# Kernel tuning notes

Hardware: AMD Instinct MI355X
Metric: run time of the kernel (lower is better)

Reference implementation:

```python
import jax, jax.numpy as jnp
import numpy as np


def setup_inputs() -> dict:
    key = jax.random.key(0)
    ks = jax.random.split(key, 8)
    B, C, H, W, D = 2, 128, 16, 16, 16
    C8 = C // 8
    return {
        "x": jax.random.normal(ks[0], (B, C, H, W, D), dtype=jnp.float32),
        "wq": jax.random.normal(ks[1], (C8, C), dtype=jnp.float32) * (1.0 / np.sqrt(C)),
        "bq": jax.random.normal(ks[2], (C8,), dtype=jnp.float32) * 0.02,
        "wk": jax.random.normal(ks[3], (C8, C), dtype=jnp.float32) * (1.0 / np.sqrt(C)),
        "bk": jax.random.normal(ks[4], (C8,), dtype=jnp.float32) * 0.02,
        "wv": jax.random.normal(ks[5], (C, C), dtype=jnp.float32) * (1.0 / np.sqrt(C)),
        "bv": jax.random.normal(ks[6], (C,), dtype=jnp.float32) * 0.02,
        "gamma": jax.random.normal(ks[7], (1,), dtype=jnp.float32) * 0.1,
    }


def reference(x, wq, bq, wk, bk, wv, bv, gamma):
    B, C, H, W, D = x.shape
    N = H * W * D
    xf = x.reshape(B, C, N)                      # (B, C, N) flatten H,W,D
    # 1x1x1 convs == per-voxel linear over channels
    q = jnp.einsum('oc,bcn->bon', wq, xf) + bq[None, :, None]   # (B, C//8, N)
    k = jnp.einsum('oc,bcn->bon', wk, xf) + bk[None, :, None]   # (B, C//8, N)
    v = jnp.einsum('oc,bcn->bon', wv, xf) + bv[None, :, None]   # (B, C, N)
    # energy[b, i, j] = sum_c q[b,c,i] * k[b,c,j]  (no scaling, as in source)
    energy = jnp.einsum('bci,bcj->bij', q, k)                   # (B, N, N)
    attn = jax.nn.softmax(energy, axis=-1)
    # out[b,c,i] = sum_j v[b,c,j] * attn[b,i,j]
    out = jnp.einsum('bcj,bij->bci', v, attn)                   # (B, C, N)
    out = out.reshape(B, C, H, W, D)
    return gamma[0] * out + x
```

## Files before the change

kernel.cpp:

```cpp
#include <hip/hip_runtime.h>
#include <hip/hip_bf16.h>
#include <math.h>

#define N_VOX 4096

typedef __bf16 bf16x8 __attribute__((ext_vector_type(8)));
typedef __bf16 bf16x4 __attribute__((ext_vector_type(4)));
typedef float f32x4 __attribute__((ext_vector_type(4)));

#define QT_OFF  0
#define KT_OFF  524288
#define VP_OFF  1048576

#define P_LN8 2.0794415f

__device__ __forceinline__ f32x4 mfma16(f32x4 a, f32x4 b, f32x4 c) {
  return __builtin_amdgcn_mfma_f32_16x16x32_bf16(
      __builtin_bit_cast(bf16x8, a), __builtin_bit_cast(bf16x8, b), c, 0, 0, 0);
}
__device__ __forceinline__ void pin(f32x4& v) { asm volatile("" : "+v"(v)); }
__device__ __forceinline__ void pinl(long& v) { asm volatile("" : "+v"(v)); }

__device__ __forceinline__ unsigned f32_to_fp8x4(float a, float b, float c, float d) {
  int v = __builtin_amdgcn_cvt_pk_fp8_f32(a, b, 0, false);
  v = __builtin_amdgcn_cvt_pk_fp8_f32(c, d, v, true);
  return (unsigned)v;
}
__device__ __forceinline__ unsigned char f32_to_fp8(float a) {
  return (unsigned char)(__builtin_amdgcn_cvt_pk_fp8_f32(a, a, 0, false) & 0xff);
}

__global__ __launch_bounds__(256) void proj_kernel(
    const float* __restrict__ x,
    const float* __restrict__ wq, const float* __restrict__ bq,
    const float* __restrict__ wk, const float* __restrict__ bk,
    const float* __restrict__ wv, const float* __restrict__ bv,
    unsigned char* __restrict__ ws8) {
  __shared__ __bf16 xs[32 * 136];
  __shared__ __bf16 wb[160 * 136];

  const int t   = threadIdx.x;
  const int bid = blockIdx.x;
  const int b   = bid >> 7;
  const int n0  = (bid & 127) * 32;

  for (int i = t; i < 5120; i += 256) {
    int gid = i * 4;
    const float* src = (gid < 2048) ? wq + gid
                     : (gid < 4096) ? wk + (gid - 2048)
                                    : wv + (gid - 4096);
    float4 f = *reinterpret_cast<const float4*>(src);
    int r = gid >> 7, col = gid & 127;
    bf16x4 o;
    o[0] = (__bf16)f.x; o[1] = (__bf16)f.y; o[2] = (__bf16)f.z; o[3] = (__bf16)f.w;
    *reinterpret_cast<bf16x4*>(&wb[r * 136 + col]) = o;
  }
  for (int idx = t; idx < 128 * 8; idx += 256) {
    int c = idx >> 3, v4 = idx & 7;
    float4 xv = *reinterpret_cast<const float4*>(
        x + (size_t)(b * 128 + c) * N_VOX + n0 + v4 * 4);
    xs[(v4 * 4 + 0) * 136 + c] = (__bf16)xv.x;
    xs[(v4 * 4 + 1) * 136 + c] = (__bf16)xv.y;
    xs[(v4 * 4 + 2) * 136 + c] = (__bf16)xv.z;
    xs[(v4 * 4 + 3) * 136 + c] = (__bf16)xv.w;
  }
  __syncthreads();

  const int w = t >> 6, lane = t & 63;
  const int cq = lane & 15, g = lane >> 4, g8 = g * 8, g4 = g * 4;

  __bf16* qt = reinterpret_cast<__bf16*>(ws8 + QT_OFF);
  __bf16* kt = reinterpret_cast<__bf16*>(ws8 + KT_OFF);
  unsigned char* vp = ws8 + VP_OFF;
  const f32x4 zero4 = {0.f, 0.f, 0.f, 0.f};

  for (int ot = w; ot < 10; ot += 4) {
    int wrow = (ot == 0) ? cq : (ot == 1) ? 16 + cq : 32 + (ot - 2) * 16 + cq;
    const float* bias = (ot == 0) ? bq : (ot == 1) ? bk : bv + (ot - 2) * 16;

    f32x4 acc[2] = {zero4, zero4};
#pragma unroll
    for (int ks = 0; ks < 4; ++ks) {
      bf16x8 af = *reinterpret_cast<const bf16x8*>(&wb[wrow * 136 + ks * 32 + g8]);
#pragma unroll
      for (int nf = 0; nf < 2; ++nf) {
        bf16x8 bfr = *reinterpret_cast<const bf16x8*>(
            &xs[(nf * 16 + cq) * 136 + ks * 32 + g8]);
        acc[nf] = __builtin_amdgcn_mfma_f32_16x16x32_bf16(af, bfr, acc[nf], 0, 0, 0);
      }
    }

    float4 bl = *reinterpret_cast<const float4*>(bias + g4);
    const float* blp = reinterpret_cast<const float*>(&bl);
#pragma unroll
    for (int nf = 0; nf < 2; ++nf) {
      int n = n0 + nf * 16 + cq;
#pragma unroll
      for (int v = 0; v < 4; ++v) {
        float val = acc[nf][v] + blp[v];
        int o = g4 + v;
        if (ot == 0) {
          qt[(size_t)(b * 4096 + n) * 32 + o] = (__bf16)val;
          qt[(size_t)(b * 4096 + n) * 32 + 16 + o] = (__bf16)0.f;
        } else if (ot == 1) {
          kt[(size_t)(b * 4096 + n) * 32 + o] = (__bf16)val;
          kt[(size_t)(b * 4096 + n) * 32 + 16 + o] = (__bf16)0.f;
        } else {
          int c  = (ot - 2) * 16 + o;
          int jt = n >> 6, j_in = n & 63;
          int cn = j_in >> 5, gg = (j_in & 31) >> 3, e = j_in & 7;
          int lt = (c & 15) | (gg << 4);
          vp[((((size_t)b * 64 + jt) * 8 + (c >> 4)) * 2 + cn) * 512 + lt * 8 + e]
              = f32_to_fp8(val);
        }
      }
    }
  }
}

__global__ __launch_bounds__(512, 2) void attn_kernel(
    const unsigned char* __restrict__ ws8,
    const float* __restrict__ x,
    const float* __restrict__ gamma_p,
    float* __restrict__ out) {
  __shared__ __align__(16) unsigned char ps[8][32 * 72];
  __shared__ float o_lds[4][128][33];
  __shared__ float m_lds[8][32], l_lds[8][32], lstar_lds[32];

  const int t    = threadIdx.x;
  const int w    = t >> 6;
  const int lane = t & 63;
  const int cq   = lane & 15;
  const int g    = lane >> 4;
  const int g8   = g * 8;
  const int g4   = g * 4;

  const int raw = blockIdx.x;
  const int xcd = raw & 7;
  const int b   = xcd >> 2;
  const int qt0 = ((raw >> 3) * 4 + (xcd & 3)) * 32;

  const __bf16* qt = reinterpret_cast<const __bf16*>(ws8 + QT_OFF);
  const __bf16* kt = reinterpret_cast<const __bf16*>(ws8 + KT_OFF);
  const unsigned char* vp = ws8 + VP_OFF;

  f32x4 qfrag[2];
#pragma unroll
  for (int qf = 0; qf < 2; ++qf)
    qfrag[qf] = *reinterpret_cast<const f32x4*>(
        qt + (size_t)(b * 4096 + qt0 + qf * 16 + cq) * 32 + g8);

  const f32x4 zero4 = {0.f, 0.f, 0.f, 0.f};
  f32x4 acc[8][2];
#pragma unroll
  for (int ct = 0; ct < 8; ++ct) { acc[ct][0] = zero4; acc[ct][1] = zero4; }
  float m0 = -1e30f, m1 = -1e30f, l0 = 0.f, l1 = 0.f;

  unsigned char* psw0 = &ps[w][cq * 72];
  unsigned char* psw1 = &ps[w][(16 + cq) * 72];
  const __bf16* kbase = kt + (size_t)(b * 4096 + cq) * 32 + g8;
  const unsigned char* vbase = vp + (size_t)b * 524288 + lane * 8;

  const int jt_base = w * 8;

  f32x4 kf[4];
#pragma unroll
  for (int s = 0; s < 4; ++s)
    kf[s] = *reinterpret_cast<const f32x4*>(
        kbase + (size_t)(jt_base * 64 + s * 16) * 32);

#pragma unroll 1
  for (int tile = 0; tile < 8; ++tile) {
    const int jt = jt_base + tile;
    const int jn = jt_base + ((tile + 1) & 7);

    long vf[2][8];
#pragma unroll
    for (int cn = 0; cn < 2; ++cn)
#pragma unroll
      for (int ct = 0; ct < 8; ++ct)
        vf[cn][ct] = *reinterpret_cast<const long*>(
            vbase + ((((size_t)jt * 8 + ct) * 2 + cn) << 9));
    f32x4 kn[4];
#pragma unroll
    for (int s = 0; s < 4; ++s)
      kn[s] = *reinterpret_cast<const f32x4*>(
          kbase + (size_t)(jn * 64 + s * 16) * 32);

    f32x4 sf[4][2];
#pragma unroll
    for (int s = 0; s < 4; ++s) {
      sf[s][0] = mfma16(kf[s], qfrag[0], zero4);
      sf[s][1] = mfma16(kf[s], qfrag[1], zero4);
    }

    float tmax0 = sf[0][0][0], tmax1 = sf[0][1][0];
#pragma unroll
    for (int s = 0; s < 4; ++s)
#pragma unroll
      for (int v = 0; v < 4; ++v) {
        tmax0 = fmaxf(tmax0, sf[s][0][v]);
        tmax1 = fmaxf(tmax1, sf[s][1][v]);
      }
    tmax0 = fmaxf(tmax0, __shfl_xor(tmax0, 16));
    tmax0 = fmaxf(tmax0, __shfl_xor(tmax0, 32));
    tmax1 = fmaxf(tmax1, __shfl_xor(tmax1, 16));
    tmax1 = fmaxf(tmax1, __shfl_xor(tmax1, 32));

    if (__any((tmax0 > m0 + 8.0f) || (tmax1 > m1 + 8.0f))) {
      float m0n = fmaxf(m0, tmax0), m1n = fmaxf(m1, tmax1);
      float sc0 = __expf(m0 - m0n), sc1 = __expf(m1 - m1n);
#pragma unroll
      for (int ct = 0; ct < 8; ++ct) { acc[ct][0] *= sc0; acc[ct][1] *= sc1; }
      l0 *= sc0; l1 *= sc1;
      m0 = m0n; m1 = m1n;
    }

    float psum0 = 0.f, psum1 = 0.f;
#pragma unroll
    for (int s = 0; s < 4; ++s) {
      float p0[4], p1[4];
#pragma unroll
      for (int v = 0; v < 4; ++v) {
        p0[v] = fminf(__expf(sf[s][0][v] - m0 - P_LN8), 440.f);
        p1[v] = fminf(__expf(sf[s][1][v] - m1 - P_LN8), 440.f);
        psum0 += p0[v]; psum1 += p1[v];
      }
      *reinterpret_cast<unsigned*>(psw0 + s * 16 + g4) =
          f32_to_fp8x4(p0[0], p0[1], p0[2], p0[3]);
      *reinterpret_cast<unsigned*>(psw1 + s * 16 + g4) =
          f32_to_fp8x4(p1[0], p1[1], p1[2], p1[3]);
    }
    psum0 += __shfl_xor(psum0, 16); psum0 += __shfl_xor(psum0, 32);
    psum1 += __shfl_xor(psum1, 16); psum1 += __shfl_xor(psum1, 32);
    l0 += psum0; l1 += psum1;

#pragma unroll
    for (int cn = 0; cn < 2; ++cn)
#pragma unroll
      for (int ct = 0; ct < 8; ++ct) pinl(vf[cn][ct]);
#pragma unroll
    for (int s = 0; s < 4; ++s) pin(kn[s]);

    __builtin_amdgcn_s_setprio(1);
#pragma unroll
    for (int cn = 0; cn < 2; ++cn) {
      long pf0 = *reinterpret_cast<const long*>(psw0 + cn * 32 + g8);
      long pf1 = *reinterpret_cast<const long*>(psw1 + cn * 32 + g8);
#pragma unroll
      for (int ct = 0; ct < 8; ++ct) {
        acc[ct][0] = __builtin_amdgcn_mfma_f32_16x16x32_fp8_fp8(
            vf[cn][ct], pf0, acc[ct][0], 0, 0, 0);
        acc[ct][1] = __builtin_amdgcn_mfma_f32_16x16x32_fp8_fp8(
            vf[cn][ct], pf1, acc[ct][1], 0, 0, 0);
      }
    }
    __builtin_amdgcn_s_setprio(0);

#pragma unroll
    for (int s = 0; s < 4; ++s) kf[s] = kn[s];
  }

  if (lane < 16) {
    m_lds[w][cq] = m0; m_lds[w][16 + cq] = m1;
    l_lds[w][cq] = l0; l_lds[w][16 + cq] = l1;
  }
  __syncthreads();

  float mstar0 = m_lds[0][cq],      mstar1 = m_lds[0][16 + cq];
#pragma unroll
  for (int ww = 1; ww < 8; ++ww) {
    mstar0 = fmaxf(mstar0, m_lds[ww][cq]);
    mstar1 = fmaxf(mstar1, m_lds[ww][16 + cq]);
  }
  float lstar0 = 0.f, lstar1 = 0.f;
#pragma unroll
  for (int ww = 0; ww < 8; ++ww) {
    lstar0 += l_lds[ww][cq]      * __expf(m_lds[ww][cq]      - mstar0);
    lstar1 += l_lds[ww][16 + cq] * __expf(m_lds[ww][16 + cq] - mstar1);
  }
  float sc0 = __expf(m0 - mstar0), sc1 = __expf(m1 - mstar1);
  if (w == 0 && lane < 16) { lstar_lds[cq] = lstar0; lstar_lds[16 + cq] = lstar1; }

  const int r = w & 3;
  if (w < 4) {
#pragma unroll
    for (int ct = 0; ct < 8; ++ct)
#pragma unroll
      for (int v = 0; v < 4; ++v) {
        o_lds[r][ct * 16 + g4 + v][cq]      = acc[ct][0][v] * sc0;
        o_lds[r][ct * 16 + g4 + v][16 + cq] = acc[ct][1][v] * sc1;
      }
  }
  __syncthreads();
  if (w >= 4) {
#pragma unroll
    for (int ct = 0; ct < 8; ++ct)
#pragma unroll
      for (int v = 0; v < 4; ++v) {
        o_lds[r][ct * 16 + g4 + v][cq]      += acc[ct][0][v] * sc0;
        o_lds[r][ct * 16 + g4 + v][16 + cq] += acc[ct][1][v] * sc1;
      }
  }
  __syncthreads();

  const float g0 = gamma_p[0];
  for (int idx = t; idx < 128 * 32; idx += 512) {
    int c = idx >> 5, qq = idx & 31;
    float o = (o_lds[0][c][qq] + o_lds[1][c][qq] +
               o_lds[2][c][qq] + o_lds[3][c][qq]) / lstar_lds[qq];
    size_t addr = (size_t)(b * 128 + c) * N_VOX + qt0 + qq;
    out[addr] = fmaf(g0, o, x[addr]);
  }
}

extern "C" void kernel_launch(void* const* d_in, const int* in_sizes, int n_in,
                              void* d_out, int out_size, void* d_ws, size_t ws_size,
                              hipStream_t stream) {
  const float* x     = (const float*)d_in[0];
  const float* wq    = (const float*)d_in[1];
  const float* bq    = (const float*)d_in[2];
  const float* wk    = (const float*)d_in[3];
  const float* bk    = (const float*)d_in[4];
  const float* wv    = (const float*)d_in[5];
  const float* bv    = (const float*)d_in[6];
  const float* gamma = (const float*)d_in[7];
  float* out = (float*)d_out;
  unsigned char* ws8 = (unsigned char*)d_ws;

  proj_kernel<<<256, 256, 0, stream>>>(x, wq, bq, wk, bk, wv, bv, ws8);
  attn_kernel<<<256, 512, 0, stream>>>(ws8, x, gamma, out);
}
```

Baseline: 34.66 us.

## Pipeline QK MFMA one tile ahead, use exp2 softmax, drop LDS weight staging

The attention loop now computes the next tile's QK scores during the current tile, overlapping them with the softmax and PV MFMAs, and prefetches K two tiles ahead. Q is pre-scaled by log2(e) so the softmax uses exp2 without the extra offset and clamp. The projection kernel reads weights directly from global memory and converts them in registers instead of staging all weights into LDS. This raises register pressure and removes the fp8 overflow clamp, which risks numerical saturation.

```diff
diff --git a/kernel.cpp b/kernel.cpp
--- a/kernel.cpp
+++ b/kernel.cpp
@@ -3,6 +3,7 @@
 #include <math.h>
 
 #define N_VOX 4096
+#define LOG2E 1.44269504f
 
 typedef __bf16 bf16x8 __attribute__((ext_vector_type(8)));
 typedef __bf16 bf16x4 __attribute__((ext_vector_type(4)));
@@ -11,8 +12,6 @@
 #define QT_OFF  0
 #define KT_OFF  524288
 #define VP_OFF  1048576
-
-#define P_LN8 2.0794415f
 
 __device__ __forceinline__ f32x4 mfma16(f32x4 a, f32x4 b, f32x4 c) {
   return __builtin_amdgcn_mfma_f32_16x16x32_bf16(
@@ -37,24 +36,12 @@
     const float* __restrict__ wv, const float* __restrict__ bv,
     unsigned char* __restrict__ ws8) {
   __shared__ __bf16 xs[32 * 136];
-  __shared__ __bf16 wb[160 * 136];
 
   const int t   = threadIdx.x;
   const int bid = blockIdx.x;
   const int b   = bid >> 7;
   const int n0  = (bid & 127) * 32;
 
-  for (int i = t; i < 5120; i += 256) {
-    int gid = i * 4;
-    const float* src = (gid < 2048) ? wq + gid
-                     : (gid < 4096) ? wk + (gid - 2048)
-                                    : wv + (gid - 4096);
-    float4 f = *reinterpret_cast<const float4*>(src);
-    int r = gid >> 7, col = gid & 127;
-    bf16x4 o;
-    o[0] = (__bf16)f.x; o[1] = (__bf16)f.y; o[2] = (__bf16)f.z; o[3] = (__bf16)f.w;
-    *reinterpret_cast<bf16x4*>(&wb[r * 136 + col]) = o;
-  }
   for (int idx = t; idx < 128 * 8; idx += 256) {
     int c = idx >> 3, v4 = idx & 7;
     float4 xv = *reinterpret_cast<const float4*>(
@@ -75,13 +62,20 @@
   const f32x4 zero4 = {0.f, 0.f, 0.f, 0.f};
 
   for (int ot = w; ot < 10; ot += 4) {
-    int wrow = (ot == 0) ? cq : (ot == 1) ? 16 + cq : 32 + (ot - 2) * 16 + cq;
-    const float* bias = (ot == 0) ? bq : (ot == 1) ? bk : bv + (ot - 2) * 16;
+    const float* wbase = (ot == 0) ? wq : (ot == 1) ? wk : wv + (ot - 2) * 16 * 128;
+    const float* bias  = (ot == 0) ? bq : (ot == 1) ? bk : bv + (ot - 2) * 16;
+    const float* wrow  = wbase + cq * 128;
 
     f32x4 acc[2] = {zero4, zero4};
 #pragma unroll
     for (int ks = 0; ks < 4; ++ks) {
-      bf16x8 af = *reinterpret_cast<const bf16x8*>(&wb[wrow * 136 + ks * 32 + g8]);
+      float4 f0 = *reinterpret_cast<const float4*>(wrow + ks * 32 + g8);
+      float4 f1 = *reinterpret_cast<const float4*>(wrow + ks * 32 + g8 + 4);
+      bf16x8 af;
+      af[0] = (__bf16)f0.x; af[1] = (__bf16)f0.y;
+      af[2] = (__bf16)f0.z; af[3] = (__bf16)f0.w;
+      af[4] = (__bf16)f1.x; af[5] = (__bf16)f1.y;
+      af[6] = (__bf16)f1.z; af[7] = (__bf16)f1.w;
 #pragma unroll
       for (int nf = 0; nf < 2; ++nf) {
         bf16x8 bfr = *reinterpret_cast<const bf16x8*>(
@@ -100,7 +94,7 @@
         float val = acc[nf][v] + blp[v];
         int o = g4 + v;
         if (ot == 0) {
-          qt[(size_t)(b * 4096 + n) * 32 + o] = (__bf16)val;
+          qt[(size_t)(b * 4096 + n) * 32 + o] = (__bf16)(val * LOG2E);
           qt[(size_t)(b * 4096 + n) * 32 + 16 + o] = (__bf16)0.f;
         } else if (ot == 1) {
           kt[(size_t)(b * 4096 + n) * 32 + o] = (__bf16)val;
@@ -163,16 +157,28 @@
 
   const int jt_base = w * 8;
 
-  f32x4 kf[4];
+  f32x4 kf0[4], kfA[4];
 #pragma unroll
   for (int s = 0; s < 4; ++s)
-    kf[s] = *reinterpret_cast<const f32x4*>(
+    kf0[s] = *reinterpret_cast<const f32x4*>(
         kbase + (size_t)(jt_base * 64 + s * 16) * 32);
+#pragma unroll
+  for (int s = 0; s < 4; ++s)
+    kfA[s] = *reinterpret_cast<const f32x4*>(
+        kbase + (size_t)((jt_base + 1) * 64 + s * 16) * 32);
+#pragma unroll
+  for (int s = 0; s < 4; ++s) pin(kf0[s]);
+
+  f32x4 sf[4][2];
+#pragma unroll
+  for (int s = 0; s < 4; ++s) {
+    sf[s][0] = mfma16(kf0[s], qfrag[0], zero4);
+    sf[s][1] = mfma16(kf0[s], qfrag[1], zero4);
+  }
 
 #pragma unroll 1
   for (int tile = 0; tile < 8; ++tile) {
     const int jt = jt_base + tile;
-    const int jn = jt_base + ((tile + 1) & 7);
 
     long vf[2][8];
 #pragma unroll
@@ -181,18 +187,12 @@
       for (int ct = 0; ct < 8; ++ct)
         vf[cn][ct] = *reinterpret_cast<const long*>(
             vbase + ((((size_t)jt * 8 + ct) * 2 + cn) << 9));
-    f32x4 kn[4];
+    f32x4 kfB[4];
+    const int j2 = jt_base + ((tile + 2) & 7);
 #pragma unroll
     for (int s = 0; s < 4; ++s)
-      kn[s] = *reinterpret_cast<const f32x4*>(
-          kbase + (size_t)(jn * 64 + s * 16) * 32);
-
-    f32x4 sf[4][2];
-#pragma unroll
-    for (int s = 0; s < 4; ++s) {
-      sf[s][0] = mfma16(kf[s], qfrag[0], zero4);
-      sf[s][1] = mfma16(kf[s], qfrag[1], zero4);
-    }
+      kfB[s] = *reinterpret_cast<const f32x4*>(
+          kbase + (size_t)(j2 * 64 + s * 16) * 32);
 
     float tmax0 = sf[0][0][0], tmax1 = sf[0][1][0];
 #pragma unroll
@@ -209,7 +209,7 @@
 
     if (__any((tmax0 > m0 + 8.0f) || (tmax1 > m1 + 8.0f))) {
       float m0n = fmaxf(m0, tmax0), m1n = fmaxf(m1, tmax1);
-      float sc0 = __expf(m0 - m0n), sc1 = __expf(m1 - m1n);
+      float sc0 = exp2f(m0 - m0n), sc1 = exp2f(m1 - m1n);
 #pragma unroll
       for (int ct = 0; ct < 8; ++ct) { acc[ct][0] *= sc0; acc[ct][1] *= sc1; }
       l0 *= sc0; l1 *= sc1;
@@ -222,8 +222,8 @@
       float p0[4], p1[4];
 #pragma unroll
       for (int v = 0; v < 4; ++v) {
-        p0[v] = fminf(__expf(sf[s][0][v] - m0 - P_LN8), 440.f);
-        p1[v] = fminf(__expf(sf[s][1][v] - m1 - P_LN8), 440.f);
+        p0[v] = exp2f(sf[s][0][v] - m0);
+        p1[v] = exp2f(sf[s][1][v] - m1);
         psum0 += p0[v]; psum1 += p1[v];
       }
       *reinterpret_cast<unsigned*>(psw0 + s * 16 + g4) =
@@ -235,12 +235,20 @@
     psum1 += __shfl_xor(psum1, 16); psum1 += __shfl_xor(psum1, 32);
     l0 += psum0; l1 += psum1;
 
+    if (tile < 7) {
+#pragma unroll
+      for (int s = 0; s < 4; ++s) pin(kfA[s]);
+#pragma unroll
+      for (int s = 0; s < 4; ++s) {
+        sf[s][0] = mfma16(kfA[s], qfrag[0], zero4);
+        sf[s][1] = mfma16(kfA[s], qfrag[1], zero4);
+      }
+    }
+
 #pragma unroll
     for (int cn = 0; cn < 2; ++cn)
 #pragma unroll
       for (int ct = 0; ct < 8; ++ct) pinl(vf[cn][ct]);
-#pragma unroll
-    for (int s = 0; s < 4; ++s) pin(kn[s]);
 
     __builtin_amdgcn_s_setprio(1);
 #pragma unroll
@@ -258,7 +266,7 @@
     __builtin_amdgcn_s_setprio(0);
 
 #pragma unroll
-    for (int s = 0; s < 4; ++s) kf[s] = kn[s];
+    for (int s = 0; s < 4; ++s) kfA[s] = kfB[s];
   }
 
   if (lane < 16) {
@@ -276,10 +284,10 @@
   float lstar0 = 0.f, lstar1 = 0.f;
 #pragma unroll
   for (int ww = 0; ww < 8; ++ww) {
-    lstar0 += l_lds[ww][cq]      * __expf(m_lds[ww][cq]      - mstar0);
-    lstar1 += l_lds[ww][16 + cq] * __expf(m_lds[ww][16 + cq] - mstar1);
-  }
-  float sc0 = __expf(m0 - mstar0), sc1 = __expf(m1 - mstar1);
+    lstar0 += l_lds[ww][cq]      * exp2f(m_lds[ww][cq]      - mstar0);
+    lstar1 += l_lds[ww][16 + cq] * exp2f(m_lds[ww][16 + cq] - mstar1);
+  }
+  float sc0 = exp2f(m0 - mstar0), sc1 = exp2f(m1 - mstar1);
   if (w == 0 && lane < 16) { lstar_lds[cq] = lstar0; lstar_lds[16 + cq] = lstar1; }
 
   const int r = w & 3;
```

Result: slower. 35.98 us (+3.8%).

## Switch attention to 32x32 MFMA with register-shuffled P fragments, no LDS

Applied to the files above, without the earlier changes.

Replaces the 16x16 MFMA tiling with 32x32x16 bf16 and fp8 MFMAs, so each wave handles 32 queries through one accumulator set of 4 f32x16. The P matrix moves from the QK accumulator layout into the PV operand layout through cross-half lane shuffles instead of an LDS round trip. Q/K storage drops the zero padding to 16 channels and V is repacked for the new fragment layout. The aim is fewer MFMA issues, no LDS traffic on the P path, and half the Q/K bytes, at the cost of more register pressure and shuffle instructions.

```diff
diff --git a/kernel.cpp b/kernel.cpp
--- a/kernel.cpp
+++ b/kernel.cpp
@@ -3,23 +3,25 @@
 #include <math.h>
 
 #define N_VOX 4096
-
+#define P_LN8 2.0794415f
+
+typedef __bf16 bf16x4 __attribute__((ext_vector_type(4)));
 typedef __bf16 bf16x8 __attribute__((ext_vector_type(8)));
-typedef __bf16 bf16x4 __attribute__((ext_vector_type(4)));
 typedef float f32x4 __attribute__((ext_vector_type(4)));
-
-#define QT_OFF  0
-#define KT_OFF  524288
-#define VP_OFF  1048576
-
-#define P_LN8 2.0794415f
-
-__device__ __forceinline__ f32x4 mfma16(f32x4 a, f32x4 b, f32x4 c) {
-  return __builtin_amdgcn_mfma_f32_16x16x32_bf16(
-      __builtin_bit_cast(bf16x8, a), __builtin_bit_cast(bf16x8, b), c, 0, 0, 0);
-}
-__device__ __forceinline__ void pin(f32x4& v) { asm volatile("" : "+v"(v)); }
+typedef float f32x16 __attribute__((ext_vector_type(16)));
+
+#define QT_OFF 0
+#define KT_OFF 262144
+#define VP_OFF 524288
+
+__device__ __forceinline__ f32x16 mfma32_bf16(bf16x8 a, bf16x8 b, f32x16 c) {
+  return __builtin_amdgcn_mfma_f32_32x32x16_bf16(a, b, c, 0, 0, 0);
+}
+__device__ __forceinline__ f32x16 mfma32_fp8(long a, long b, f32x16 c) {
+  return __builtin_amdgcn_mfma_f32_32x32x16_fp8_fp8(a, b, c, 0, 0, 0);
+}
 __device__ __forceinline__ void pinl(long& v) { asm volatile("" : "+v"(v)); }
+__device__ __forceinline__ void pinb(bf16x8& v) { asm volatile("" : "+v"(v)); }
 
 __device__ __forceinline__ unsigned f32_to_fp8x4(float a, float b, float c, float d) {
   int v = __builtin_amdgcn_cvt_pk_fp8_f32(a, b, 0, false);
@@ -95,23 +97,19 @@
 #pragma unroll
     for (int nf = 0; nf < 2; ++nf) {
       int n = n0 + nf * 16 + cq;
-#pragma unroll
-      for (int v = 0; v < 4; ++v) {
-        float val = acc[nf][v] + blp[v];
-        int o = g4 + v;
-        if (ot == 0) {
-          qt[(size_t)(b * 4096 + n) * 32 + o] = (__bf16)val;
-          qt[(size_t)(b * 4096 + n) * 32 + 16 + o] = (__bf16)0.f;
-        } else if (ot == 1) {
-          kt[(size_t)(b * 4096 + n) * 32 + o] = (__bf16)val;
-          kt[(size_t)(b * 4096 + n) * 32 + 16 + o] = (__bf16)0.f;
-        } else {
-          int c  = (ot - 2) * 16 + o;
-          int jt = n >> 6, j_in = n & 63;
-          int cn = j_in >> 5, gg = (j_in & 31) >> 3, e = j_in & 7;
-          int lt = (c & 15) | (gg << 4);
-          vp[((((size_t)b * 64 + jt) * 8 + (c >> 4)) * 2 + cn) * 512 + lt * 8 + e]
-              = f32_to_fp8(val);
+      if (ot < 2) {
+        bf16x4 pk;
+#pragma unroll
+        for (int v = 0; v < 4; ++v) pk[v] = (__bf16)(acc[nf][v] + blp[v]);
+        __bf16* dst = (ot == 0) ? qt : kt;
+        *reinterpret_cast<bf16x4*>(dst + (size_t)(b * 4096 + n) * 16 + g4) = pk;
+      } else {
+#pragma unroll
+        for (int v = 0; v < 4; ++v) {
+          float val = acc[nf][v] + blp[v];
+          int c = (ot - 2) * 16 + g4 + v;
+          vp[(((size_t)(b * 256 + (n >> 4)) * 4 + (c >> 5)) << 9)
+             + (((n >> 3) & 1) * 32 + (c & 31)) * 8 + (n & 7)] = f32_to_fp8(val);
         }
       }
     }
@@ -123,17 +121,14 @@
     const float* __restrict__ x,
     const float* __restrict__ gamma_p,
     float* __restrict__ out) {
-  __shared__ __align__(16) unsigned char ps[8][32 * 72];
   __shared__ float o_lds[4][128][33];
   __shared__ float m_lds[8][32], l_lds[8][32], lstar_lds[32];
 
   const int t    = threadIdx.x;
   const int w    = t >> 6;
   const int lane = t & 63;
-  const int cq   = lane & 15;
-  const int g    = lane >> 4;
-  const int g8   = g * 8;
-  const int g4   = g * 4;
+  const int l31  = lane & 31;
+  const int hi   = lane >> 5;
 
   const int raw = blockIdx.x;
   const int xcd = raw & 7;
@@ -144,163 +139,140 @@
   const __bf16* kt = reinterpret_cast<const __bf16*>(ws8 + KT_OFF);
   const unsigned char* vp = ws8 + VP_OFF;
 
-  f32x4 qfrag[2];
-#pragma unroll
-  for (int qf = 0; qf < 2; ++qf)
-    qfrag[qf] = *reinterpret_cast<const f32x4*>(
-        qt + (size_t)(b * 4096 + qt0 + qf * 16 + cq) * 32 + g8);
-
-  const f32x4 zero4 = {0.f, 0.f, 0.f, 0.f};
-  f32x4 acc[8][2];
-#pragma unroll
-  for (int ct = 0; ct < 8; ++ct) { acc[ct][0] = zero4; acc[ct][1] = zero4; }
-  float m0 = -1e30f, m1 = -1e30f, l0 = 0.f, l1 = 0.f;
-
-  unsigned char* psw0 = &ps[w][cq * 72];
-  unsigned char* psw1 = &ps[w][(16 + cq) * 72];
-  const __bf16* kbase = kt + (size_t)(b * 4096 + cq) * 32 + g8;
+  bf16x8 qf = *reinterpret_cast<const bf16x8*>(
+      qt + (size_t)(b * 4096 + qt0 + l31) * 16 + hi * 8);
+
+  f32x16 acc[4];
+#pragma unroll
+  for (int cb = 0; cb < 4; ++cb)
+#pragma unroll
+    for (int r = 0; r < 16; ++r) acc[cb][r] = 0.f;
+  const f32x16 zero16 = acc[0];
+  float m = -1e30f, l = 0.f;
+
+  const __bf16* kbase = kt + (size_t)(b * 4096 + l31) * 16 + hi * 8;
   const unsigned char* vbase = vp + (size_t)b * 524288 + lane * 8;
 
   const int jt_base = w * 8;
 
-  f32x4 kf[4];
-#pragma unroll
-  for (int s = 0; s < 4; ++s)
-    kf[s] = *reinterpret_cast<const f32x4*>(
-        kbase + (size_t)(jt_base * 64 + s * 16) * 32);
+  bf16x8 kf0 = *reinterpret_cast<const bf16x8*>(kbase + (size_t)(jt_base * 64) * 16);
+  bf16x8 kf1 = *reinterpret_cast<const bf16x8*>(kbase + (size_t)(jt_base * 64 + 32) * 16);
 
 #pragma unroll 1
   for (int tile = 0; tile < 8; ++tile) {
     const int jt = jt_base + tile;
-    const int jn = jt_base + ((tile + 1) & 7);
-
-    long vf[2][8];
-#pragma unroll
-    for (int cn = 0; cn < 2; ++cn)
-#pragma unroll
-      for (int ct = 0; ct < 8; ++ct)
-        vf[cn][ct] = *reinterpret_cast<const long*>(
-            vbase + ((((size_t)jt * 8 + ct) * 2 + cn) << 9));
-    f32x4 kn[4];
-#pragma unroll
-    for (int s = 0; s < 4; ++s)
-      kn[s] = *reinterpret_cast<const f32x4*>(
-          kbase + (size_t)(jn * 64 + s * 16) * 32);
-
-    f32x4 sf[4][2];
-#pragma unroll
-    for (int s = 0; s < 4; ++s) {
-      sf[s][0] = mfma16(kf[s], qfrag[0], zero4);
-      sf[s][1] = mfma16(kf[s], qfrag[1], zero4);
-    }
-
-    float tmax0 = sf[0][0][0], tmax1 = sf[0][1][0];
-#pragma unroll
-    for (int s = 0; s < 4; ++s)
-#pragma unroll
-      for (int v = 0; v < 4; ++v) {
-        tmax0 = fmaxf(tmax0, sf[s][0][v]);
-        tmax1 = fmaxf(tmax1, sf[s][1][v]);
+    const int jtn = jt_base + ((tile + 1) & 7);
+
+    long vf[4][4];
+#pragma unroll
+    for (int jc = 0; jc < 4; ++jc)
+#pragma unroll
+      for (int cb = 0; cb < 4; ++cb)
+        vf[jc][cb] = *reinterpret_cast<const long*>(
+            vbase + (((size_t)(jt * 4 + jc) * 4 + cb) << 9));
+    bf16x8 kn0 = *reinterpret_cast<const bf16x8*>(kbase + (size_t)(jtn * 64) * 16);
+    bf16x8 kn1 = *reinterpret_cast<const bf16x8*>(kbase + (size_t)(jtn * 64 + 32) * 16);
+
+    f32x16 sf0 = mfma32_bf16(kf0, qf, zero16);
+    f32x16 sf1 = mfma32_bf16(kf1, qf, zero16);
+
+    float tmax = sf0[0];
+#pragma unroll
+    for (int r = 1; r < 16; ++r) tmax = fmaxf(tmax, sf0[r]);
+#pragma unroll
+    for (int r = 0; r < 16; ++r) tmax = fmaxf(tmax, sf1[r]);
+    tmax = fmaxf(tmax, __shfl_xor(tmax, 32));
+
+    if (__any(tmax > m + 8.0f)) {
+      float mn = fmaxf(m, tmax);
+      float sc = __expf(m - mn);
+#pragma unroll
+      for (int cb = 0; cb < 4; ++cb)
+#pragma unroll
+        for (int r = 0; r < 16; ++r) acc[cb][r] *= sc;
+      l *= sc;
+      m = mn;
+    }
+
+    float p0[16], p1[16];
+    float psum = 0.f;
+#pragma unroll
+    for (int r = 0; r < 16; ++r) {
+      p0[r] = fminf(__expf(sf0[r] - m - P_LN8), 440.f);
+      p1[r] = fminf(__expf(sf1[r] - m - P_LN8), 440.f);
+      psum += p0[r] + p1[r];
+    }
+    psum += __shfl_xor(psum, 32);
+    l += psum;
+
+    unsigned W0[4], W1[4], X0[4], X1[4];
+#pragma unroll
+    for (int i = 0; i < 4; ++i) {
+      W0[i] = f32_to_fp8x4(p0[4 * i], p0[4 * i + 1], p0[4 * i + 2], p0[4 * i + 3]);
+      W1[i] = f32_to_fp8x4(p1[4 * i], p1[4 * i + 1], p1[4 * i + 2], p1[4 * i + 3]);
+    }
+#pragma unroll
+    for (int i = 0; i < 4; ++i) {
+      X0[i] = __shfl_xor(W0[i], 32);
+      X1[i] = __shfl_xor(W1[i], 32);
+    }
+
+#pragma unroll
+    for (int jc = 0; jc < 4; ++jc)
+#pragma unroll
+      for (int cb = 0; cb < 4; ++cb) pinl(vf[jc][cb]);
+    pinb(kn0); pinb(kn1);
+
+    __builtin_amdgcn_s_setprio(1);
+#pragma unroll
+    for (int jc = 0; jc < 4; ++jc) {
+      const int pb = (jc & 1) * 2;
+      unsigned wd0, wd1;
+      if (jc < 2) {
+        wd0 = hi ? X0[pb + 1] : W0[pb];
+        wd1 = hi ? W0[pb + 1] : X0[pb];
+      } else {
+        wd0 = hi ? X1[pb + 1] : W1[pb];
+        wd1 = hi ? W1[pb + 1] : X1[pb];
       }
-    tmax0 = fmaxf(tmax0, __shfl_xor(tmax0, 16));
-    tmax0 = fmaxf(tmax0, __shfl_xor(tmax0, 32));
-    tmax1 = fmaxf(tmax1, __shfl_xor(tmax1, 16));
-    tmax1 = fmaxf(tmax1, __shfl_xor(tmax1, 32));
-
-    if (__any((tmax0 > m0 + 8.0f) || (tmax1 > m1 + 8.0f))) {
-      float m0n = fmaxf(m0, tmax0), m1n = fmaxf(m1, tmax1);
-      float sc0 = __expf(m0 - m0n), sc1 = __expf(m1 - m1n);
-#pragma unroll
-      for (int ct = 0; ct < 8; ++ct) { acc[ct][0] *= sc0; acc[ct][1] *= sc1; }
-      l0 *= sc0; l1 *= sc1;
-      m0 = m0n; m1 = m1n;
-    }
-
-    float psum0 = 0.f, psum1 = 0.f;
-#pragma unroll
-    for (int s = 0; s < 4; ++s) {
-      float p0[4], p1[4];
-#pragma unroll
-      for (int v = 0; v < 4; ++v) {
-        p0[v] = fminf(__expf(sf[s][0][v] - m0 - P_LN8), 440.f);
-        p1[v] = fminf(__expf(sf[s][1][v] - m1 - P_LN8), 440.f);
-        psum0 += p0[v]; psum1 += p1[v];
-      }
-      *reinterpret_cast<unsigned*>(psw0 + s * 16 + g4) =
-          f32_to_fp8x4(p0[0], p0[1], p0[2], p0[3]);
-      *reinterpret_cast<unsigned*>(psw1 + s * 16 + g4) =
-          f32_to_fp8x4(p1[0], p1[1], p1[2], p1[3]);
-    }
-    psum0 += __shfl_xor(psum0, 16); psum0 += __shfl_xor(psum0, 32);
-    psum1 += __shfl_xor(psum1, 16); psum1 += __shfl_xor(psum1, 32);
-    l0 += psum0; l1 += psum1;
-
-#pragma unroll
-    for (int cn = 0; cn < 2; ++cn)
-#pragma unroll
-      for (int ct = 0; ct < 8; ++ct) pinl(vf[cn][ct]);
-#pragma unroll
-    for (int s = 0; s < 4; ++s) pin(kn[s]);
-
-    __builtin_amdgcn_s_setprio(1);
-#pragma unroll
-    for (int cn = 0; cn < 2; ++cn) {
-      long pf0 = *reinterpret_cast<const long*>(psw0 + cn * 32 + g8);
-      long pf1 = *reinterpret_cast<const long*>(psw1 + cn * 32 + g8);
-#pragma unroll
-      for (int ct = 0; ct < 8; ++ct) {
-        acc[ct][0] = __builtin_amdgcn_mfma_f32_16x16x32_fp8_fp8(
-            vf[cn][ct], pf0, acc[ct][0], 0, 0, 0);
-        acc[ct][1] = __builtin_amdgcn_mfma_f32_16x16x32_fp8_fp8(
-            vf[cn][ct], pf1, acc[ct][1], 0, 0, 0);
-      }
+      long pf = (long)(((unsigned long long)wd1 << 32) | wd0);
+#pragma unroll
+      for (int cb = 0; cb < 4; ++cb)
+        acc[cb] = mfma32_fp8(vf[jc][cb], pf, acc[cb]);
     }
     __builtin_amdgcn_s_setprio(0);
 
-#pragma unroll
-    for (int s = 0; s < 4; ++s) kf[s] = kn[s];
-  }
-
-  if (lane < 16) {
-    m_lds[w][cq] = m0; m_lds[w][16 + cq] = m1;
-    l_lds[w][cq] = l0; l_lds[w][16 + cq] = l1;
-  }
+    kf0 = kn0; kf1 = kn1;
+  }
+
+  if (lane < 32) { m_lds[w][lane] = m; l_lds[w][lane] = l; }
   __syncthreads();
 
-  float mstar0 = m_lds[0][cq],      mstar1 = m_lds[0][16 + cq];
-#pragma unroll
-  for (int ww = 1; ww < 8; ++ww) {
-    mstar0 = fmaxf(mstar0, m_lds[ww][cq]);
-    mstar1 = fmaxf(mstar1, m_lds[ww][16 + cq]);
-  }
-  float lstar0 = 0.f, lstar1 = 0.f;
-#pragma unroll
-  for (int ww = 0; ww < 8; ++ww) {
-    lstar0 += l_lds[ww][cq]      * __expf(m_lds[ww][cq]      - mstar0);
-    lstar1 += l_lds[ww][16 + cq] * __expf(m_lds[ww][16 + cq] - mstar1);
-  }
-  float sc0 = __expf(m0 - mstar0), sc1 = __expf(m1 - mstar1);
-  if (w == 0 && lane < 16) { lstar_lds[cq] = lstar0; lstar_lds[16 + cq] = lstar1; }
-
-  const int r = w & 3;
+  float mstar = m_lds[0][l31];
+#pragma unroll
+  for (int ww = 1; ww < 8; ++ww) mstar = fmaxf(mstar, m_lds[ww][l31]);
+  float lstar = 0.f;
+#pragma unroll
+  for (int ww = 0; ww < 8; ++ww)
+    lstar += l_lds[ww][l31] * __expf(m_lds[ww][l31] - mstar);
+  float sc = __expf(m - mstar);
+  if (w == 0 && lane < 32) lstar_lds[lane] = lstar;
+
+  const int rr = w & 3;
   if (w < 4) {
 #pragma unroll
-    for (int ct = 0; ct < 8; ++ct)
-#pragma unroll
-      for (int v = 0; v < 4; ++v) {
-        o_lds[r][ct * 16 + g4 + v][cq]      = acc[ct][0][v] * sc0;
-        o_lds[r][ct * 16 + g4 + v][16 + cq] = acc[ct][1][v] * sc1;
-      }
+    for (int cb = 0; cb < 4; ++cb)
+#pragma unroll
+      for (int r = 0; r < 16; ++r)
+        o_lds[rr][cb * 32 + (r & 3) + 8 * (r >> 2) + 4 * hi][l31] = acc[cb][r] * sc;
   }
   __syncthreads();
   if (w >= 4) {
 #pragma unroll
-    for (int ct = 0; ct < 8; ++ct)
-#pragma unroll
-      for (int v = 0; v < 4; ++v) {
-        o_lds[r][ct * 16 + g4 + v][cq]      += acc[ct][0][v] * sc0;
-        o_lds[r][ct * 16 + g4 + v][16 + cq] += acc[ct][1][v] * sc1;
-      }
+    for (int cb = 0; cb < 4; ++cb)
+#pragma unroll
+      for (int r = 0; r < 16; ++r)
+        o_lds[rr][cb * 32 + (r & 3) + 8 * (r >> 2) + 4 * hi][l31] += acc[cb][r] * sc;
   }
   __syncthreads();
 
```

New measurement: 31.85 us. -8.1%, faster.
